# Performance work log

Measured on AMD Instinct MI355X. Metric: run time of the kernel, lower is better.

The kernel has to match this reference:

```python
import jax, jax.numpy as jnp
import numpy as np

S, B, V, E, H = 512, 256, 100000, 128, 256


def setup_inputs() -> dict:
    key = jax.random.key(0)
    k1, k2, k3, k4, k5, k6 = jax.random.split(key, 6)
    X = jax.random.randint(k1, (S, B), 0, V)
    emb = jax.random.normal(k2, (V, E), dtype=jnp.float32)
    # PyTorch nn.RNN init: U(-1/sqrt(H), 1/sqrt(H))
    s = 1.0 / np.sqrt(H)
    W_ih = jax.random.uniform(k3, (H, E), minval=-s, maxval=s, dtype=jnp.float32)
    W_hh = jax.random.uniform(k4, (H, H), minval=-s, maxval=s, dtype=jnp.float32)
    b_ih = jax.random.uniform(k5, (H,), minval=-s, maxval=s, dtype=jnp.float32)
    b_hh = jax.random.uniform(k6, (H,), minval=-s, maxval=s, dtype=jnp.float32)
    return {"X": X, "emb": emb, "W_ih": W_ih, "W_hh": W_hh, "b_ih": b_ih, "b_hh": b_hh}


def reference(X, emb, W_ih, W_hh, b_ih, b_hh):
    embedded = emb[X]                                   # [S, B, E]
    # Precompute input projections for all timesteps (one big GEMM)
    xproj = jnp.einsum('sbe,he->sbh', embedded, W_ih) + b_ih + b_hh  # [S, B, H]
    h0 = jnp.zeros((B, H), dtype=embedded.dtype)

    def step(h, xp):
        h_new = jnp.tanh(xp + h @ W_hh.T)
        return h_new, None

    h_last, _ = jax.lax.scan(step, h0, xproj)           # [B, H]
    return jax.nn.log_softmax(h_last, axis=1)
```

## Files before the change

kernel.cpp:

```cpp
#include <hip/hip_runtime.h>
#include <math.h>

#define S_LEN 512
#define B_SZ  256
#define E_SZ  128
#define H_SZ  256

typedef __attribute__((ext_vector_type(8))) short bf16x8;
typedef __attribute__((ext_vector_type(4))) short bf16x4;
typedef __attribute__((ext_vector_type(4))) float f32x4;

__device__ __forceinline__ short f2bf(float f) {
    union { float f; unsigned u; } v; v.f = f;
    unsigned r = v.u + 0x7FFFu + ((v.u >> 16) & 1u);
    return (short)(r >> 16);
}
__device__ __forceinline__ float bf2f(short h) {
    union { unsigned u; float f; } c;
    c.u = ((unsigned)(unsigned short)h) << 16;
    return c.f;
}

__device__ __forceinline__ float tanh_fast(float v) {
    float e = __expf(2.f * v);
    return 1.f - 2.f * __builtin_amdgcn_rcpf(e + 1.f);
}

__global__ __launch_bounds__(256, 2) void embed_proj_mfma(
    const int*   __restrict__ X,
    const float* __restrict__ emb,
    const float* __restrict__ W_ih,
    const float* __restrict__ b_ih,
    const float* __restrict__ b_hh,
    float*       __restrict__ xproj)
{
    __shared__ int   toks[64];
    __shared__ short BtH[4][4][64][8];
    __shared__ short BtL[4][4][64][8];

    const int tid  = threadIdx.x;
    const int wave = tid >> 6;
    const int lane = tid & 63;
    const int bl   = lane & 15;
    const int quad = lane >> 4;
    const size_t row0 = (size_t)blockIdx.x * 64;

    if (tid < 64) toks[tid] = X[row0 + tid];
    __syncthreads();

    {
        const int r  = tid >> 2;
        const int kk = tid & 3;
        const float* ep = emb + (size_t)toks[r] * E_SZ + kk * 32;
#pragma unroll
        for (int q = 0; q < 4; ++q) {
            float4 a = *(const float4*)(ep + q * 8);
            float4 b = *(const float4*)(ep + q * 8 + 4);
            float v[8] = {a.x, a.y, a.z, a.w, b.x, b.y, b.z, b.w};
            bf16x8 fh, fl;
#pragma unroll
            for (int j = 0; j < 8; ++j) {
                short h = f2bf(v[j]);
                fh[j] = h;
                fl[j] = f2bf(v[j] - bf2f(h));
            }
            *(bf16x8*)&BtH[r >> 4][kk][q * 16 + (r & 15)][0] = fh;
            *(bf16x8*)&BtL[r >> 4][kk][q * 16 + (r & 15)][0] = fl;
        }
    }
    __syncthreads();

#pragma unroll
    for (int mp = 0; mp < 2; ++mp) {
        bf16x8 wh[2][4], wl[2][4];
#pragma unroll
        for (int i = 0; i < 2; ++i) {
            const int h = wave * 64 + (mp * 2 + i) * 16 + bl;
#pragma unroll
            for (int kk = 0; kk < 4; ++kk) {
                const float* wp = W_ih + (size_t)h * E_SZ + kk * 32 + quad * 8;
                float4 a = *(const float4*)wp;
                float4 b = *(const float4*)(wp + 4);
                float v[8] = {a.x, a.y, a.z, a.w, b.x, b.y, b.z, b.w};
                bf16x8 fh, fl;
#pragma unroll
                for (int j = 0; j < 8; ++j) {
                    short hh = f2bf(v[j]);
                    fh[j] = hh;
                    fl[j] = f2bf(v[j] - bf2f(hh));
                }
                wh[i][kk] = fh; wl[i][kk] = fl;
            }
        }

        f32x4 acc[2][4];
#pragma unroll
        for (int i = 0; i < 2; ++i)
#pragma unroll
            for (int nt = 0; nt < 4; ++nt) acc[i][nt] = (f32x4){0.f, 0.f, 0.f, 0.f};

#pragma unroll
        for (int kk = 0; kk < 4; ++kk) {
            bf16x8 bh[4], blo[4];
#pragma unroll
            for (int nt = 0; nt < 4; ++nt) {
                bh[nt]  = *(const bf16x8*)&BtH[nt][kk][lane][0];
                blo[nt] = *(const bf16x8*)&BtL[nt][kk][lane][0];
            }
#pragma unroll
            for (int i = 0; i < 2; ++i)
#pragma unroll
                for (int nt = 0; nt < 4; ++nt) {
                    f32x4 a = acc[i][nt];
                    a = __builtin_amdgcn_mfma_f32_16x16x32_bf16(wh[i][kk], bh[nt],  a, 0, 0, 0);
                    a = __builtin_amdgcn_mfma_f32_16x16x32_bf16(wh[i][kk], blo[nt], a, 0, 0, 0);
                    a = __builtin_amdgcn_mfma_f32_16x16x32_bf16(wl[i][kk], bh[nt],  a, 0, 0, 0);
                    acc[i][nt] = a;
                }
        }

#pragma unroll
        for (int i = 0; i < 2; ++i) {
            const int hb = wave * 64 + (mp * 2 + i) * 16 + quad * 4;
            float4 bi = *(const float4*)&b_ih[hb];
            float4 bh4 = *(const float4*)&b_hh[hb];
#pragma unroll
            for (int nt = 0; nt < 4; ++nt) {
                f32x4 o = acc[i][nt];
                o[0] += bi.x + bh4.x; o[1] += bi.y + bh4.y;
                o[2] += bi.z + bh4.z; o[3] += bi.w + bh4.w;
                *(f32x4*)&xproj[(row0 + nt * 16 + bl) * H_SZ + hb] = o;
            }
        }
    }
}

__global__ __launch_bounds__(512) void rnn_scan_kernel(
    const float* __restrict__ xproj,
    const float* __restrict__ W_hh,
    float*       __restrict__ out)
{
    const int tid  = threadIdx.x;
    const int wave = tid >> 6;
    const int lane = tid & 63;
    const int bl   = lane & 15;
    const int quad = lane >> 4;
    const int B0   = blockIdx.x * 16;

    __shared__ short HB[2][8][64][8];
    __shared__ float sred[8][16];

    bf16x8 wfrag[2][8];
#pragma unroll
    for (int mt = 0; mt < 2; ++mt) {
        const int h = wave * 32 + mt * 16 + bl;
#pragma unroll
        for (int kk = 0; kk < 8; ++kk) {
            const float* wp = W_hh + (size_t)h * H_SZ + kk * 32 + quad * 8;
            float4 x0 = *(const float4*)wp;
            float4 x1 = *(const float4*)(wp + 4);
            bf16x8 f;
            f[0] = f2bf(x0.x); f[1] = f2bf(x0.y); f[2] = f2bf(x0.z); f[3] = f2bf(x0.w);
            f[4] = f2bf(x1.x); f[5] = f2bf(x1.y); f[6] = f2bf(x1.z); f[7] = f2bf(x1.w);
            wfrag[mt][kk] = f;
        }
    }

    short* const hb0 = &HB[0][0][0][0];
    short* const hb1 = &HB[1][0][0][0];

    ((int4*)hb0)[tid] = make_int4(0, 0, 0, 0);

    const short* rd0 = hb0 + lane * 8;
    const short* rd1 = hb1 + lane * 8;

    const int wo0 = wave * 512 + (quad >> 1) * 128 + bl * 8 + (quad & 1) * 4;
    const int wo1 = wo0 + 256;
    short* w0a = hb0 + wo0; short* w0b = hb0 + wo1;
    short* w1a = hb1 + wo0; short* w1b = hb1 + wo1;

    const size_t stp = (size_t)B_SZ * H_SZ;
    const float* xpb = xproj + (size_t)(B0 + bl) * H_SZ + wave * 32 + quad * 4;

    f32x4 xA0 = *(const f32x4*)(xpb);
    f32x4 xA1 = *(const f32x4*)(xpb + 16);
    f32x4 xB0 = *(const f32x4*)(xpb + stp);
    f32x4 xB1 = *(const f32x4*)(xpb + stp + 16);

    __syncthreads();

    float vf0[4], vf1[4];

    auto do_step = [&](const short* rd, short* wa, short* wb,
                       f32x4& x0, f32x4& x1, const float* pf) {
        bf16x8 bf[8];
#pragma unroll
        for (int kk = 0; kk < 8; ++kk)
            bf[kk] = *(const bf16x8*)(rd + kk * 512);

        f32x4 c0a = {0.f, 0.f, 0.f, 0.f}, c0b = {0.f, 0.f, 0.f, 0.f};
        f32x4 c1a = {0.f, 0.f, 0.f, 0.f}, c1b = {0.f, 0.f, 0.f, 0.f};
#pragma unroll
        for (int kk = 0; kk < 4; ++kk) {
            c0a = __builtin_amdgcn_mfma_f32_16x16x32_bf16(wfrag[0][kk],     bf[kk],     c0a, 0, 0, 0);
            c1a = __builtin_amdgcn_mfma_f32_16x16x32_bf16(wfrag[1][kk],     bf[kk],     c1a, 0, 0, 0);
            c0b = __builtin_amdgcn_mfma_f32_16x16x32_bf16(wfrag[0][kk + 4], bf[kk + 4], c0b, 0, 0, 0);
            c1b = __builtin_amdgcn_mfma_f32_16x16x32_bf16(wfrag[1][kk + 4], bf[kk + 4], c1b, 0, 0, 0);
        }
        const f32x4 d0 = c0a + c0b;
        const f32x4 d1 = c1a + c1b;

        float t0 = tanh_fast(d0[0] + x0[0]);
        float t1 = tanh_fast(d0[1] + x0[1]);
        float t2 = tanh_fast(d0[2] + x0[2]);
        float t3 = tanh_fast(d0[3] + x0[3]);
        float u0 = tanh_fast(d1[0] + x1[0]);
        float u1 = tanh_fast(d1[1] + x1[1]);
        float u2 = tanh_fast(d1[2] + x1[2]);
        float u3 = tanh_fast(d1[3] + x1[3]);
        unsigned p01, p23, q01, q23;
        asm("v_cvt_pk_bf16_f32 %0, %1, %2" : "=v"(p01) : "v"(t0), "v"(t1));
        asm("v_cvt_pk_bf16_f32 %0, %1, %2" : "=v"(p23) : "v"(t2), "v"(t3));
        asm("v_cvt_pk_bf16_f32 %0, %1, %2" : "=v"(q01) : "v"(u0), "v"(u1));
        asm("v_cvt_pk_bf16_f32 %0, %1, %2" : "=v"(q23) : "v"(u2), "v"(u3));
        *(uint2*)wa = make_uint2(p01, p23);
        *(uint2*)wb = make_uint2(q01, q23);

        x0 = *(const f32x4*)pf;
        x1 = *(const f32x4*)(pf + 16);

        asm volatile("s_waitcnt lgkmcnt(0)" ::: "memory");
        __builtin_amdgcn_sched_barrier(0);
        __builtin_amdgcn_s_barrier();
    };

    const float* pfA = xpb + 2 * stp;
    const float* pfB = xpb + 3 * stp;
    for (int s = 0; s < 510; s += 2) {
        do_step(rd0, w1a, w1b, xA0, xA1, pfA);
        do_step(rd1, w0a, w0b, xB0, xB1, pfB);
        pfA += 2 * stp; pfB += 2 * stp;
        if (pfA > xpb + 511 * stp) pfA = xpb;
        if (pfB > xpb + 511 * stp) pfB = xpb;
    }
    do_step(rd0, w1a, w1b, xA0, xA1, xpb);

    {
        bf16x8 bf[8];
#pragma unroll
        for (int kk = 0; kk < 8; ++kk)
            bf[kk] = *(const bf16x8*)(rd1 + kk * 512);
        f32x4 c0a = {0.f, 0.f, 0.f, 0.f}, c0b = {0.f, 0.f, 0.f, 0.f};
        f32x4 c1a = {0.f, 0.f, 0.f, 0.f}, c1b = {0.f, 0.f, 0.f, 0.f};
#pragma unroll
        for (int kk = 0; kk < 4; ++kk) {
            c0a = __builtin_amdgcn_mfma_f32_16x16x32_bf16(wfrag[0][kk],     bf[kk],     c0a, 0, 0, 0);
            c1a = __builtin_amdgcn_mfma_f32_16x16x32_bf16(wfrag[1][kk],     bf[kk],     c1a, 0, 0, 0);
            c0b = __builtin_amdgcn_mfma_f32_16x16x32_bf16(wfrag[0][kk + 4], bf[kk + 4], c0b, 0, 0, 0);
            c1b = __builtin_amdgcn_mfma_f32_16x16x32_bf16(wfrag[1][kk + 4], bf[kk + 4], c1b, 0, 0, 0);
        }
        const f32x4 d0 = c0a + c0b;
        const f32x4 d1 = c1a + c1b;
#pragma unroll
        for (int r = 0; r < 4; ++r) {
            vf0[r] = tanh_fast(d0[r] + xB0[r]);
            vf1[r] = tanh_fast(d1[r] + xB1[r]);
        }
    }

    float m = fmaxf(fmaxf(fmaxf(vf0[0], vf0[1]), fmaxf(vf0[2], vf0[3])),
                    fmaxf(fmaxf(vf1[0], vf1[1]), fmaxf(vf1[2], vf1[3])));
    m = fmaxf(m, __shfl_xor(m, 16));
    m = fmaxf(m, __shfl_xor(m, 32));
    if (lane < 16) sred[wave][bl] = m;
    __syncthreads();
    float mall = sred[0][bl];
#pragma unroll
    for (int w = 1; w < 8; ++w) mall = fmaxf(mall, sred[w][bl]);
    __syncthreads();

    float ss = 0.f;
#pragma unroll
    for (int r = 0; r < 4; ++r)
        ss += __expf(vf0[r] - mall) + __expf(vf1[r] - mall);
    ss += __shfl_xor(ss, 16);
    ss += __shfl_xor(ss, 32);
    if (lane < 16) sred[wave][bl] = ss;
    __syncthreads();
    float tot = sred[0][bl];
#pragma unroll
    for (int w = 1; w < 8; ++w) tot += sred[w][bl];
    const float lse = mall + __logf(tot);

    f32x4 o0, o1;
#pragma unroll
    for (int r = 0; r < 4; ++r) { o0[r] = vf0[r] - lse; o1[r] = vf1[r] - lse; }
    float* op = out + (size_t)(B0 + bl) * H_SZ + wave * 32 + quad * 4;
    *(f32x4*)op        = o0;
    *(f32x4*)(op + 16) = o1;
}

extern "C" void kernel_launch(void* const* d_in, const int* in_sizes, int n_in,
                              void* d_out, int out_size, void* d_ws, size_t ws_size,
                              hipStream_t stream) {
    const int*   X    = (const int*)  d_in[0];
    const float* emb  = (const float*)d_in[1];
    const float* W_ih = (const float*)d_in[2];
    const float* W_hh = (const float*)d_in[3];
    const float* b_ih = (const float*)d_in[4];
    const float* b_hh = (const float*)d_in[5];
    float* out   = (float*)d_out;
    float* xproj = (float*)d_ws;

    embed_proj_mfma<<<dim3((S_LEN * B_SZ) / 64), 256, 0, stream>>>(
        X, emb, W_ih, b_ih, b_hh, xproj);

    rnn_scan_kernel<<<dim3(B_SZ / 16), 512, 0, stream>>>(xproj, W_hh, out);
}
```

Baseline: 464.1 us.

## Pre-split W_ih to bf16 hi/lo, drop LDS staging, and halve scan block waves

```diff
diff --git a/kernel.cpp b/kernel.cpp
--- a/kernel.cpp
+++ b/kernel.cpp
@@ -7,18 +7,32 @@
 #define H_SZ  256
 
 typedef __attribute__((ext_vector_type(8))) short bf16x8;
-typedef __attribute__((ext_vector_type(4))) short bf16x4;
 typedef __attribute__((ext_vector_type(4))) float f32x4;
 
-__device__ __forceinline__ short f2bf(float f) {
-    union { float f; unsigned u; } v; v.f = f;
-    unsigned r = v.u + 0x7FFFu + ((v.u >> 16) & 1u);
-    return (short)(r >> 16);
-}
-__device__ __forceinline__ float bf2f(short h) {
-    union { unsigned u; float f; } c;
-    c.u = ((unsigned)(unsigned short)h) << 16;
-    return c.f;
+__device__ short g_wh[H_SZ * E_SZ];
+__device__ short g_wl[H_SZ * E_SZ];
+
+__device__ __forceinline__ unsigned pkbf(float a, float b) {
+    unsigned r; asm("v_cvt_pk_bf16_f32 %0, %1, %2" : "=v"(r) : "v"(a), "v"(b));
+    return r;
+}
+__device__ __forceinline__ float fromlo(unsigned u) {
+    union { unsigned u; float f; } c; c.u = u << 16; return c.f;
+}
+__device__ __forceinline__ float fromhi(unsigned u) {
+    union { unsigned u; float f; } c; c.u = u & 0xffff0000u; return c.f;
+}
+__device__ __forceinline__ void cvt_hilo8(float4 a, float4 b, bf16x8& hi, bf16x8& lo) {
+    unsigned h0 = pkbf(a.x, a.y), h1 = pkbf(a.z, a.w);
+    unsigned h2 = pkbf(b.x, b.y), h3 = pkbf(b.z, b.w);
+    unsigned l0 = pkbf(a.x - fromlo(h0), a.y - fromhi(h0));
+    unsigned l1 = pkbf(a.z - fromlo(h1), a.w - fromhi(h1));
+    unsigned l2 = pkbf(b.x - fromlo(h2), b.y - fromhi(h2));
+    unsigned l3 = pkbf(b.z - fromlo(h3), b.w - fromhi(h3));
+    union { bf16x8 v; unsigned u[4]; } H, L;
+    H.u[0] = h0; H.u[1] = h1; H.u[2] = h2; H.u[3] = h3;
+    L.u[0] = l0; L.u[1] = l1; L.u[2] = l2; L.u[3] = l3;
+    hi = H.v; lo = L.v;
 }
 
 __device__ __forceinline__ float tanh_fast(float v) {
@@ -26,18 +40,23 @@
     return 1.f - 2.f * __builtin_amdgcn_rcpf(e + 1.f);
 }
 
+__global__ void prep_w_kernel(const float* __restrict__ W_ih) {
+    const int i = (blockIdx.x * 256 + threadIdx.x) * 8;
+    float4 a = *(const float4*)&W_ih[i];
+    float4 b = *(const float4*)&W_ih[i + 4];
+    bf16x8 h, l;
+    cvt_hilo8(a, b, h, l);
+    *(bf16x8*)&g_wh[i] = h;
+    *(bf16x8*)&g_wl[i] = l;
+}
+
 __global__ __launch_bounds__(256, 2) void embed_proj_mfma(
     const int*   __restrict__ X,
     const float* __restrict__ emb,
-    const float* __restrict__ W_ih,
     const float* __restrict__ b_ih,
     const float* __restrict__ b_hh,
     float*       __restrict__ xproj)
 {
-    __shared__ int   toks[64];
-    __shared__ short BtH[4][4][64][8];
-    __shared__ short BtL[4][4][64][8];
-
     const int tid  = threadIdx.x;
     const int wave = tid >> 6;
     const int lane = tid & 63;
@@ -45,97 +64,68 @@
     const int quad = lane >> 4;
     const size_t row0 = (size_t)blockIdx.x * 64;
 
-    if (tid < 64) toks[tid] = X[row0 + tid];
-    __syncthreads();
-
-    {
-        const int r  = tid >> 2;
-        const int kk = tid & 3;
-        const float* ep = emb + (size_t)toks[r] * E_SZ + kk * 32;
-#pragma unroll
-        for (int q = 0; q < 4; ++q) {
-            float4 a = *(const float4*)(ep + q * 8);
-            float4 b = *(const float4*)(ep + q * 8 + 4);
-            float v[8] = {a.x, a.y, a.z, a.w, b.x, b.y, b.z, b.w};
-            bf16x8 fh, fl;
-#pragma unroll
-            for (int j = 0; j < 8; ++j) {
-                short h = f2bf(v[j]);
-                fh[j] = h;
-                fl[j] = f2bf(v[j] - bf2f(h));
+    int tok[4];
+#pragma unroll
+    for (int nt = 0; nt < 4; ++nt) tok[nt] = X[row0 + nt * 16 + bl];
+
+    bf16x8 wh[4][4], wl[4][4];
+#pragma unroll
+    for (int mt = 0; mt < 4; ++mt) {
+        const int off0 = (wave * 64 + mt * 16 + bl) * E_SZ + quad * 8;
+#pragma unroll
+        for (int kk = 0; kk < 4; ++kk) {
+            wh[mt][kk] = *(const bf16x8*)&g_wh[off0 + kk * 32];
+            wl[mt][kk] = *(const bf16x8*)&g_wl[off0 + kk * 32];
+        }
+    }
+
+    f32x4 bias[4];
+#pragma unroll
+    for (int mt = 0; mt < 4; ++mt) {
+        const int hb = wave * 64 + mt * 16 + quad * 4;
+        float4 bi = *(const float4*)&b_ih[hb];
+        float4 bh = *(const float4*)&b_hh[hb];
+        bias[mt][0] = bi.x + bh.x; bias[mt][1] = bi.y + bh.y;
+        bias[mt][2] = bi.z + bh.z; bias[mt][3] = bi.w + bh.w;
+    }
+
+#pragma unroll
+    for (int nt = 0; nt < 4; ++nt) {
+        const float* ep = emb + (size_t)tok[nt] * E_SZ + quad * 8;
+        bf16x8 bh8[4], bl8[4];
+#pragma unroll
+        for (int kk = 0; kk < 4; ++kk) {
+            float4 a = *(const float4*)(ep + kk * 32);
+            float4 b = *(const float4*)(ep + kk * 32 + 4);
+            cvt_hilo8(a, b, bh8[kk], bl8[kk]);
+        }
+
+        f32x4 acc[4];
+#pragma unroll
+        for (int mt = 0; mt < 4; ++mt) acc[mt] = (f32x4){0.f, 0.f, 0.f, 0.f};
+
+#pragma unroll
+        for (int kk = 0; kk < 4; ++kk)
+#pragma unroll
+            for (int mt = 0; mt < 4; ++mt) {
+                f32x4 a = acc[mt];
+                a = __builtin_amdgcn_mfma_f32_16x16x32_bf16(wh[mt][kk], bh8[kk], a, 0, 0, 0);
+                a = __builtin_amdgcn_mfma_f32_16x16x32_bf16(wh[mt][kk], bl8[kk], a, 0, 0, 0);
+                a = __builtin_amdgcn_mfma_f32_16x16x32_bf16(wl[mt][kk], bh8[kk], a, 0, 0, 0);
+                acc[mt] = a;
             }
-            *(bf16x8*)&BtH[r >> 4][kk][q * 16 + (r & 15)][0] = fh;
-            *(bf16x8*)&BtL[r >> 4][kk][q * 16 + (r & 15)][0] = fl;
-        }
-    }
-    __syncthreads();
-
-#pragma unroll
-    for (int mp = 0; mp < 2; ++mp) {
-        bf16x8 wh[2][4], wl[2][4];
-#pragma unroll
-        for (int i = 0; i < 2; ++i) {
-            const int h = wave * 64 + (mp * 2 + i) * 16 + bl;
-#pragma unroll
-            for (int kk = 0; kk < 4; ++kk) {
-                const float* wp = W_ih + (size_t)h * E_SZ + kk * 32 + quad * 8;
-                float4 a = *(const float4*)wp;
-                float4 b = *(const float4*)(wp + 4);
-                float v[8] = {a.x, a.y, a.z, a.w, b.x, b.y, b.z, b.w};
-                bf16x8 fh, fl;
-#pragma unroll
-                for (int j = 0; j < 8; ++j) {
-                    short hh = f2bf(v[j]);
-                    fh[j] = hh;
-                    fl[j] = f2bf(v[j] - bf2f(hh));
-                }
-                wh[i][kk] = fh; wl[i][kk] = fl;
-            }
-        }
-
-        f32x4 acc[2][4];
-#pragma unroll
-        for (int i = 0; i < 2; ++i)
-#pragma unroll
-            for (int nt = 0; nt < 4; ++nt) acc[i][nt] = (f32x4){0.f, 0.f, 0.f, 0.f};
-
-#pragma unroll
-        for (int kk = 0; kk < 4; ++kk) {
-            bf16x8 bh[4], blo[4];
-#pragma unroll
-            for (int nt = 0; nt < 4; ++nt) {
-                bh[nt]  = *(const bf16x8*)&BtH[nt][kk][lane][0];
-                blo[nt] = *(const bf16x8*)&BtL[nt][kk][lane][0];
-            }
-#pragma unroll
-            for (int i = 0; i < 2; ++i)
-#pragma unroll
-                for (int nt = 0; nt < 4; ++nt) {
-                    f32x4 a = acc[i][nt];
-                    a = __builtin_amdgcn_mfma_f32_16x16x32_bf16(wh[i][kk], bh[nt],  a, 0, 0, 0);
-                    a = __builtin_amdgcn_mfma_f32_16x16x32_bf16(wh[i][kk], blo[nt], a, 0, 0, 0);
-                    a = __builtin_amdgcn_mfma_f32_16x16x32_bf16(wl[i][kk], bh[nt],  a, 0, 0, 0);
-                    acc[i][nt] = a;
-                }
-        }
-
-#pragma unroll
-        for (int i = 0; i < 2; ++i) {
-            const int hb = wave * 64 + (mp * 2 + i) * 16 + quad * 4;
-            float4 bi = *(const float4*)&b_ih[hb];
-            float4 bh4 = *(const float4*)&b_hh[hb];
-#pragma unroll
-            for (int nt = 0; nt < 4; ++nt) {
-                f32x4 o = acc[i][nt];
-                o[0] += bi.x + bh4.x; o[1] += bi.y + bh4.y;
-                o[2] += bi.z + bh4.z; o[3] += bi.w + bh4.w;
-                *(f32x4*)&xproj[(row0 + nt * 16 + bl) * H_SZ + hb] = o;
-            }
-        }
-    }
-}
-
-__global__ __launch_bounds__(512) void rnn_scan_kernel(
+
+#pragma unroll
+        for (int mt = 0; mt < 4; ++mt) {
+            f32x4 o = acc[mt];
+            o[0] += bias[mt][0]; o[1] += bias[mt][1];
+            o[2] += bias[mt][2]; o[3] += bias[mt][3];
+            *(f32x4*)&xproj[(row0 + nt * 16 + bl) * H_SZ + wave * 64 + mt * 16 + quad * 4] = o;
+        }
+    }
+}
+
+__global__ __launch_bounds__(256, 1) void rnn_scan_kernel(
     const float* __restrict__ xproj,
     const float* __restrict__ W_hh,
     float*       __restrict__ out)
@@ -147,87 +137,94 @@
     const int quad = lane >> 4;
     const int B0   = blockIdx.x * 16;
 
-    __shared__ short HB[2][8][64][8];
-    __shared__ float sred[8][16];
-
-    bf16x8 wfrag[2][8];
-#pragma unroll
-    for (int mt = 0; mt < 2; ++mt) {
-        const int h = wave * 32 + mt * 16 + bl;
+    __shared__ short HB[2][4096];
+    __shared__ float sred[4][16];
+
+    bf16x8 wfrag[4][8];
+#pragma unroll
+    for (int mt = 0; mt < 4; ++mt) {
+        const int h = wave * 64 + mt * 16 + bl;
 #pragma unroll
         for (int kk = 0; kk < 8; ++kk) {
             const float* wp = W_hh + (size_t)h * H_SZ + kk * 32 + quad * 8;
-            float4 x0 = *(const float4*)wp;
-            float4 x1 = *(const float4*)(wp + 4);
-            bf16x8 f;
-            f[0] = f2bf(x0.x); f[1] = f2bf(x0.y); f[2] = f2bf(x0.z); f[3] = f2bf(x0.w);
-            f[4] = f2bf(x1.x); f[5] = f2bf(x1.y); f[6] = f2bf(x1.z); f[7] = f2bf(x1.w);
-            wfrag[mt][kk] = f;
-        }
-    }
-
-    short* const hb0 = &HB[0][0][0][0];
-    short* const hb1 = &HB[1][0][0][0];
-
-    ((int4*)hb0)[tid] = make_int4(0, 0, 0, 0);
+            float4 a = *(const float4*)wp;
+            float4 b = *(const float4*)(wp + 4);
+            union { bf16x8 v; unsigned u[4]; } F;
+            F.u[0] = pkbf(a.x, a.y); F.u[1] = pkbf(a.z, a.w);
+            F.u[2] = pkbf(b.x, b.y); F.u[3] = pkbf(b.z, b.w);
+            wfrag[mt][kk] = F.v;
+        }
+    }
+
+    short* const hb0 = HB[0];
+    short* const hb1 = HB[1];
+    ((int4*)hb0)[tid]       = make_int4(0, 0, 0, 0);
+    ((int4*)hb0)[tid + 256] = make_int4(0, 0, 0, 0);
 
     const short* rd0 = hb0 + lane * 8;
     const short* rd1 = hb1 + lane * 8;
 
-    const int wo0 = wave * 512 + (quad >> 1) * 128 + bl * 8 + (quad & 1) * 4;
-    const int wo1 = wo0 + 256;
-    short* w0a = hb0 + wo0; short* w0b = hb0 + wo1;
-    short* w1a = hb1 + wo0; short* w1b = hb1 + wo1;
+    const int wbase = wave * 1024 + (quad >> 1) * 128 + bl * 8 + (quad & 1) * 4;
+    short* const w0 = hb0 + wbase;
+    short* const w1 = hb1 + wbase;
 
     const size_t stp = (size_t)B_SZ * H_SZ;
-    const float* xpb = xproj + (size_t)(B0 + bl) * H_SZ + wave * 32 + quad * 4;
+    const float* xpb = xproj + (size_t)(B0 + bl) * H_SZ + wave * 64 + quad * 4;
 
     f32x4 xA0 = *(const f32x4*)(xpb);
     f32x4 xA1 = *(const f32x4*)(xpb + 16);
+    f32x4 xA2 = *(const f32x4*)(xpb + 32);
+    f32x4 xA3 = *(const f32x4*)(xpb + 48);
     f32x4 xB0 = *(const f32x4*)(xpb + stp);
     f32x4 xB1 = *(const f32x4*)(xpb + stp + 16);
+    f32x4 xB2 = *(const f32x4*)(xpb + stp + 32);
+    f32x4 xB3 = *(const f32x4*)(xpb + stp + 48);
 
     __syncthreads();
 
-    float vf0[4], vf1[4];
-
-    auto do_step = [&](const short* rd, short* wa, short* wb,
-                       f32x4& x0, f32x4& x1, const float* pf) {
+    auto do_step = [&](const short* rd, short* wr,
+                       f32x4& x0, f32x4& x1, f32x4& x2, f32x4& x3,
+                       const float* pf) {
         bf16x8 bf[8];
 #pragma unroll
         for (int kk = 0; kk < 8; ++kk)
             bf[kk] = *(const bf16x8*)(rd + kk * 512);
 
-        f32x4 c0a = {0.f, 0.f, 0.f, 0.f}, c0b = {0.f, 0.f, 0.f, 0.f};
-        f32x4 c1a = {0.f, 0.f, 0.f, 0.f}, c1b = {0.f, 0.f, 0.f, 0.f};
+        f32x4 ca0 = {0.f,0.f,0.f,0.f}, ca1 = {0.f,0.f,0.f,0.f};
+        f32x4 ca2 = {0.f,0.f,0.f,0.f}, ca3 = {0.f,0.f,0.f,0.f};
+        f32x4 cb0 = {0.f,0.f,0.f,0.f}, cb1 = {0.f,0.f,0.f,0.f};
+        f32x4 cb2 = {0.f,0.f,0.f,0.f}, cb3 = {0.f,0.f,0.f,0.f};
 #pragma unroll
         for (int kk = 0; kk < 4; ++kk) {
-            c0a = __builtin_amdgcn_mfma_f32_16x16x32_bf16(wfrag[0][kk],     bf[kk],     c0a, 0, 0, 0);
-            c1a = __builtin_amdgcn_mfma_f32_16x16x32_bf16(wfrag[1][kk],     bf[kk],     c1a, 0, 0, 0);
-            c0b = __builtin_amdgcn_mfma_f32_16x16x32_bf16(wfrag[0][kk + 4], bf[kk + 4], c0b, 0, 0, 0);
-            c1b = __builtin_amdgcn_mfma_f32_16x16x32_bf16(wfrag[1][kk + 4], bf[kk + 4], c1b, 0, 0, 0);
-        }
-        const f32x4 d0 = c0a + c0b;
-        const f32x4 d1 = c1a + c1b;
-
-        float t0 = tanh_fast(d0[0] + x0[0]);
-        float t1 = tanh_fast(d0[1] + x0[1]);
-        float t2 = tanh_fast(d0[2] + x0[2]);
-        float t3 = tanh_fast(d0[3] + x0[3]);
-        float u0 = tanh_fast(d1[0] + x1[0]);
-        float u1 = tanh_fast(d1[1] + x1[1]);
-        float u2 = tanh_fast(d1[2] + x1[2]);
-        float u3 = tanh_fast(d1[3] + x1[3]);
-        unsigned p01, p23, q01, q23;
-        asm("v_cvt_pk_bf16_f32 %0, %1, %2" : "=v"(p01) : "v"(t0), "v"(t1));
-        asm("v_cvt_pk_bf16_f32 %0, %1, %2" : "=v"(p23) : "v"(t2), "v"(t3));
-        asm("v_cvt_pk_bf16_f32 %0, %1, %2" : "=v"(q01) : "v"(u0), "v"(u1));
-        asm("v_cvt_pk_bf16_f32 %0, %1, %2" : "=v"(q23) : "v"(u2), "v"(u3));
-        *(uint2*)wa = make_uint2(p01, p23);
-        *(uint2*)wb = make_uint2(q01, q23);
+            ca0 = __builtin_amdgcn_mfma_f32_16x16x32_bf16(wfrag[0][kk],   bf[kk],   ca0, 0, 0, 0);
+            ca1 = __builtin_amdgcn_mfma_f32_16x16x32_bf16(wfrag[1][kk],   bf[kk],   ca1, 0, 0, 0);
+            ca2 = __builtin_amdgcn_mfma_f32_16x16x32_bf16(wfrag[2][kk],   bf[kk],   ca2, 0, 0, 0);
+            ca3 = __builtin_amdgcn_mfma_f32_16x16x32_bf16(wfrag[3][kk],   bf[kk],   ca3, 0, 0, 0);
+            cb0 = __builtin_amdgcn_mfma_f32_16x16x32_bf16(wfrag[0][kk+4], bf[kk+4], cb0, 0, 0, 0);
+            cb1 = __builtin_amdgcn_mfma_f32_16x16x32_bf16(wfrag[1][kk+4], bf[kk+4], cb1, 0, 0, 0);
+            cb2 = __builtin_amdgcn_mfma_f32_16x16x32_bf16(wfrag[2][kk+4], bf[kk+4], cb2, 0, 0, 0);
+            cb3 = __builtin_amdgcn_mfma_f32_16x16x32_bf16(wfrag[3][kk+4], bf[kk+4], cb3, 0, 0, 0);
+        }
+        const f32x4 d0 = ca0 + cb0, d1 = ca1 + cb1;
+        const f32x4 d2 = ca2 + cb2, d3 = ca3 + cb3;
+
+#define EPI(dd, xx, OFF) { \
+        float t0 = tanh_fast(dd[0] + xx[0]); \
+        float t1 = tanh_fast(dd[1] + xx[1]); \
+        float t2 = tanh_fast(dd[2] + xx[2]); \
+        float t3 = tanh_fast(dd[3] + xx[3]); \
+        unsigned pa = pkbf(t0, t1), pb = pkbf(t2, t3); \
+        *(uint2*)(wr + (OFF)) = make_uint2(pa, pb); }
+        EPI(d0, x0, 0)
+        EPI(d1, x1, 256)
+        EPI(d2, x2, 512)
+        EPI(d3, x3, 768)
+#undef EPI
 
         x0 = *(const f32x4*)pf;
         x1 = *(const f32x4*)(pf + 16);
+        x2 = *(const f32x4*)(pf + 32);
+        x3 = *(const f32x4*)(pf + 48);
 
         asm volatile("s_waitcnt lgkmcnt(0)" ::: "memory");
         __builtin_amdgcn_sched_barrier(0);
@@ -237,67 +234,79 @@
     const float* pfA = xpb + 2 * stp;
     const float* pfB = xpb + 3 * stp;
     for (int s = 0; s < 510; s += 2) {
-        do_step(rd0, w1a, w1b, xA0, xA1, pfA);
-        do_step(rd1, w0a, w0b, xB0, xB1, pfB);
+        do_step(rd0, w1, xA0, xA1, xA2, xA3, pfA);
+        do_step(rd1, w0, xB0, xB1, xB2, xB3, pfB);
         pfA += 2 * stp; pfB += 2 * stp;
         if (pfA > xpb + 511 * stp) pfA = xpb;
         if (pfB > xpb + 511 * stp) pfB = xpb;
     }
-    do_step(rd0, w1a, w1b, xA0, xA1, xpb);
-
+    do_step(rd0, w1, xA0, xA1, xA2, xA3, xpb);
+
+    float vf[4][4];
     {
         bf16x8 bf[8];
 #pragma unroll
         for (int kk = 0; kk < 8; ++kk)
             bf[kk] = *(const bf16x8*)(rd1 + kk * 512);
-        f32x4 c0a = {0.f, 0.f, 0.f, 0.f}, c0b = {0.f, 0.f, 0.f, 0.f};
-        f32x4 c1a = {0.f, 0.f, 0.f, 0.f}, c1b = {0.f, 0.f, 0.f, 0.f};
+        f32x4 ca0 = {0.f,0.f,0.f,0.f}, ca1 = {0.f,0.f,0.f,0.f};
+        f32x4 ca2 = {0.f,0.f,0.f,0.f}, ca3 = {0.f,0.f,0.f,0.f};
+        f32x4 cb0 = {0.f,0.f,0.f,0.f}, cb1 = {0.f,0.f,0.f,0.f};
+        f32x4 cb2 = {0.f,0.f,0.f,0.f}, cb3 = {0.f,0.f,0.f,0.f};
 #pragma unroll
         for (int kk = 0; kk < 4; ++kk) {
-            c0a = __builtin_amdgcn_mfma_f32_16x16x32_bf16(wfrag[0][kk],     bf[kk],     c0a, 0, 0, 0);
-            c1a = __builtin_amdgcn_mfma_f32_16x16x32_bf16(wfrag[1][kk],     bf[kk],     c1a, 0, 0, 0);
-            c0b = __builtin_amdgcn_mfma_f32_16x16x32_bf16(wfrag[0][kk + 4], bf[kk + 4], c0b, 0, 0, 0);
-            c1b = __builtin_amdgcn_mfma_f32_16x16x32_bf16(wfrag[1][kk + 4], bf[kk + 4], c1b, 0, 0, 0);
-        }
-        const f32x4 d0 = c0a + c0b;
-        const f32x4 d1 = c1a + c1b;
+            ca0 = __builtin_amdgcn_mfma_f32_16x16x32_bf16(wfrag[0][kk],   bf[kk],   ca0, 0, 0, 0);
+            ca1 = __builtin_amdgcn_mfma_f32_16x16x32_bf16(wfrag[1][kk],   bf[kk],   ca1, 0, 0, 0);
+            ca2 = __builtin_amdgcn_mfma_f32_16x16x32_bf16(wfrag[2][kk],   bf[kk],   ca2, 0, 0, 0);
+            ca3 = __builtin_amdgcn_mfma_f32_16x16x32_bf16(wfrag[3][kk],   bf[kk],   ca3, 0, 0, 0);
+            cb0 = __builtin_amdgcn_mfma_f32_16x16x32_bf16(wfrag[0][kk+4], bf[kk+4], cb0, 0, 0, 0);
+            cb1 = __builtin_amdgcn_mfma_f32_16x16x32_bf16(wfrag[1][kk+4], bf[kk+4], cb1, 0, 0, 0);
+            cb2 = __builtin_amdgcn_mfma_f32_16x16x32_bf16(wfrag[2][kk+4], bf[kk+4], cb2, 0, 0, 0);
+            cb3 = __builtin_amdgcn_mfma_f32_16x16x32_bf16(wfrag[3][kk+4], bf[kk+4], cb3, 0, 0, 0);
+        }
+        const f32x4 d0 = ca0 + cb0, d1 = ca1 + cb1;
+        const f32x4 d2 = ca2 + cb2, d3 = ca3 + cb3;
 #pragma unroll
         for (int r = 0; r < 4; ++r) {
-            vf0[r] = tanh_fast(d0[r] + xB0[r]);
-            vf1[r] = tanh_fast(d1[r] + xB1[r]);
-        }
-    }
-
-    float m = fmaxf(fmaxf(fmaxf(vf0[0], vf0[1]), fmaxf(vf0[2], vf0[3])),
-                    fmaxf(fmaxf(vf1[0], vf1[1]), fmaxf(vf1[2], vf1[3])));
+            vf[0][r] = tanh_fast(d0[r] + xB0[r]);
+            vf[1][r] = tanh_fast(d1[r] + xB1[r]);
+            vf[2][r] = tanh_fast(d2[r] + xB2[r]);
+            vf[3][r] = tanh_fast(d3[r] + xB3[r]);
+        }
+    }
+
+    float m = -1e30f;
+#pragma unroll
+    for (int mt = 0; mt < 4; ++mt)
+#pragma unroll
+        for (int r = 0; r < 4; ++r) m = fmaxf(m, vf[mt][r]);
     m = fmaxf(m, __shfl_xor(m, 16));
     m = fmaxf(m, __shfl_xor(m, 32));
     if (lane < 16) sred[wave][bl] = m;
     __syncthreads();
-    float mall = sred[0][bl];
-#pragma unroll
-    for (int w = 1; w < 8; ++w) mall = fmaxf(mall, sred[w][bl]);
+    const float mall = fmaxf(fmaxf(sred[0][bl], sred[1][bl]),
+                             fmaxf(sred[2][bl], sred[3][bl]));
     __syncthreads();
 
     float ss = 0.f;
 #pragma unroll
-    for (int r = 0; r < 4; ++r)
-        ss += __expf(vf0[r] - mall) + __expf(vf1[r] - mall);
+    for (int mt = 0; mt < 4; ++mt)
+#pragma unroll
+        for (int r = 0; r < 4; ++r) ss += __expf(vf[mt][r] - mall);
     ss += __shfl_xor(ss, 16);
     ss += __shfl_xor(ss, 32);
     if (lane < 16) sred[wave][bl] = ss;
     __syncthreads();
-    float tot = sred[0][bl];
-#pragma unroll
-    for (int w = 1; w < 8; ++w) tot += sred[w][bl];
+    const float tot = sred[0][bl] + sred[1][bl] + sred[2][bl] + sred[3][bl];
     const float lse = mall + __logf(tot);
 
-    f32x4 o0, o1;
-#pragma unroll
-    for (int r = 0; r < 4; ++r) { o0[r] = vf0[r] - lse; o1[r] = vf1[r] - lse; }
-    float* op = out + (size_t)(B0 + bl) * H_SZ + wave * 32 + quad * 4;
-    *(f32x4*)op        = o0;
-    *(f32x4*)(op + 16) = o1;
+    float* op = out + (size_t)(B0 + bl) * H_SZ + wave * 64 + quad * 4;
+#pragma unroll
+    for (int mt = 0; mt < 4; ++mt) {
+        f32x4 o;
+#pragma unroll
+        for (int r = 0; r < 4; ++r) o[r] = vf[mt][r] - lse;
+        *(f32x4*)(op + mt * 16) = o;
+    }
 }
 
 extern "C" void kernel_launch(void* const* d_in, const int* in_sizes, int n_in,
@@ -312,8 +321,8 @@
     float* out   = (float*)d_out;
     float* xproj = (float*)d_ws;
 
+    prep_w_kernel<<<dim3(16), 256, 0, stream>>>(W_ih);
     embed_proj_mfma<<<dim3((S_LEN * B_SZ) / 64), 256, 0, stream>>>(
-        X, emb, W_ih, b_ih, b_hh, xproj);
-
-    rnn_scan_kernel<<<dim3(B_SZ / 16), 512, 0, stream>>>(xproj, W_hh, out);
-}
+        X, emb, b_ih, b_hh, xproj);
+    rnn_scan_kernel<<<dim3(B_SZ / 16), 256, 0, stream>>>(xproj, W_hh, out);
+}
```

Result: slower. 557.9 us (+20.2%).

## Precompute bf16 hi/lo W_ih split, use packed converts, and shorten scan step chain

Applied to the files above, without the earlier changes.

```diff
diff --git a/kernel.cpp b/kernel.cpp
--- a/kernel.cpp
+++ b/kernel.cpp
@@ -7,29 +7,52 @@
 #define H_SZ  256
 
 typedef __attribute__((ext_vector_type(8))) short bf16x8;
-typedef __attribute__((ext_vector_type(4))) short bf16x4;
 typedef __attribute__((ext_vector_type(4))) float f32x4;
 
-__device__ __forceinline__ short f2bf(float f) {
-    union { float f; unsigned u; } v; v.f = f;
-    unsigned r = v.u + 0x7FFFu + ((v.u >> 16) & 1u);
-    return (short)(r >> 16);
-}
-__device__ __forceinline__ float bf2f(short h) {
-    union { unsigned u; float f; } c;
-    c.u = ((unsigned)(unsigned short)h) << 16;
-    return c.f;
-}
-
-__device__ __forceinline__ float tanh_fast(float v) {
-    float e = __expf(2.f * v);
-    return 1.f - 2.f * __builtin_amdgcn_rcpf(e + 1.f);
+__device__ short g_wh[H_SZ * E_SZ];
+__device__ short g_wl[H_SZ * E_SZ];
+
+__device__ __forceinline__ unsigned pkbf(float a, float b) {
+    unsigned r; asm("v_cvt_pk_bf16_f32 %0, %1, %2" : "=v"(r) : "v"(a), "v"(b));
+    return r;
+}
+__device__ __forceinline__ float fromlo(unsigned u) {
+    union { unsigned u; float f; } c; c.u = u << 16; return c.f;
+}
+__device__ __forceinline__ float fromhi(unsigned u) {
+    union { unsigned u; float f; } c; c.u = u & 0xffff0000u; return c.f;
+}
+__device__ __forceinline__ void cvt_hilo8(float4 a, float4 b, bf16x8& hi, bf16x8& lo) {
+    unsigned h0 = pkbf(a.x, a.y), h1 = pkbf(a.z, a.w);
+    unsigned h2 = pkbf(b.x, b.y), h3 = pkbf(b.z, b.w);
+    unsigned l0 = pkbf(a.x - fromlo(h0), a.y - fromhi(h0));
+    unsigned l1 = pkbf(a.z - fromlo(h1), a.w - fromhi(h1));
+    unsigned l2 = pkbf(b.x - fromlo(h2), b.y - fromhi(h2));
+    unsigned l3 = pkbf(b.z - fromlo(h3), b.w - fromhi(h3));
+    union { bf16x8 v; unsigned u[4]; } H, L;
+    H.u[0] = h0; H.u[1] = h1; H.u[2] = h2; H.u[3] = h3;
+    L.u[0] = l0; L.u[1] = l1; L.u[2] = l2; L.u[3] = l3;
+    hi = H.v; lo = L.v;
+}
+
+__device__ __forceinline__ float tanhC(float v) {
+    float e = __builtin_amdgcn_exp2f(v * 2.8853900818f);
+    return fmaf(-2.f, __builtin_amdgcn_rcpf(e + 1.f), 1.f);
+}
+
+__global__ void prep_w_kernel(const float* __restrict__ W_ih) {
+    const int i = (blockIdx.x * 256 + threadIdx.x) * 8;
+    float4 a = *(const float4*)&W_ih[i];
+    float4 b = *(const float4*)&W_ih[i + 4];
+    bf16x8 h, l;
+    cvt_hilo8(a, b, h, l);
+    *(bf16x8*)&g_wh[i] = h;
+    *(bf16x8*)&g_wl[i] = l;
 }
 
 __global__ __launch_bounds__(256, 2) void embed_proj_mfma(
     const int*   __restrict__ X,
     const float* __restrict__ emb,
-    const float* __restrict__ W_ih,
     const float* __restrict__ b_ih,
     const float* __restrict__ b_hh,
     float*       __restrict__ xproj)
@@ -56,14 +79,8 @@
         for (int q = 0; q < 4; ++q) {
             float4 a = *(const float4*)(ep + q * 8);
             float4 b = *(const float4*)(ep + q * 8 + 4);
-            float v[8] = {a.x, a.y, a.z, a.w, b.x, b.y, b.z, b.w};
             bf16x8 fh, fl;
-#pragma unroll
-            for (int j = 0; j < 8; ++j) {
-                short h = f2bf(v[j]);
-                fh[j] = h;
-                fl[j] = f2bf(v[j] - bf2f(h));
-            }
+            cvt_hilo8(a, b, fh, fl);
             *(bf16x8*)&BtH[r >> 4][kk][q * 16 + (r & 15)][0] = fh;
             *(bf16x8*)&BtL[r >> 4][kk][q * 16 + (r & 15)][0] = fl;
         }
@@ -75,21 +92,11 @@
         bf16x8 wh[2][4], wl[2][4];
 #pragma unroll
         for (int i = 0; i < 2; ++i) {
-            const int h = wave * 64 + (mp * 2 + i) * 16 + bl;
+            const int off0 = (wave * 64 + (mp * 2 + i) * 16 + bl) * E_SZ + quad * 8;
 #pragma unroll
             for (int kk = 0; kk < 4; ++kk) {
-                const float* wp = W_ih + (size_t)h * E_SZ + kk * 32 + quad * 8;
-                float4 a = *(const float4*)wp;
-                float4 b = *(const float4*)(wp + 4);
-                float v[8] = {a.x, a.y, a.z, a.w, b.x, b.y, b.z, b.w};
-                bf16x8 fh, fl;
-#pragma unroll
-                for (int j = 0; j < 8; ++j) {
-                    short hh = f2bf(v[j]);
-                    fh[j] = hh;
-                    fl[j] = f2bf(v[j] - bf2f(hh));
-                }
-                wh[i][kk] = fh; wl[i][kk] = fl;
+                wh[i][kk] = *(const bf16x8*)&g_wh[off0 + kk * 32];
+                wl[i][kk] = *(const bf16x8*)&g_wl[off0 + kk * 32];
             }
         }
 
@@ -122,7 +129,7 @@
 #pragma unroll
         for (int i = 0; i < 2; ++i) {
             const int hb = wave * 64 + (mp * 2 + i) * 16 + quad * 4;
-            float4 bi = *(const float4*)&b_ih[hb];
+            float4 bi  = *(const float4*)&b_ih[hb];
             float4 bh4 = *(const float4*)&b_hh[hb];
 #pragma unroll
             for (int nt = 0; nt < 4; ++nt) {
@@ -157,12 +164,12 @@
 #pragma unroll
         for (int kk = 0; kk < 8; ++kk) {
             const float* wp = W_hh + (size_t)h * H_SZ + kk * 32 + quad * 8;
-            float4 x0 = *(const float4*)wp;
-            float4 x1 = *(const float4*)(wp + 4);
-            bf16x8 f;
-            f[0] = f2bf(x0.x); f[1] = f2bf(x0.y); f[2] = f2bf(x0.z); f[3] = f2bf(x0.w);
-            f[4] = f2bf(x1.x); f[5] = f2bf(x1.y); f[6] = f2bf(x1.z); f[7] = f2bf(x1.w);
-            wfrag[mt][kk] = f;
+            float4 a = *(const float4*)wp;
+            float4 b = *(const float4*)(wp + 4);
+            union { bf16x8 v; unsigned u[4]; } F;
+            F.u[0] = pkbf(a.x, a.y); F.u[1] = pkbf(a.z, a.w);
+            F.u[2] = pkbf(b.x, b.y); F.u[3] = pkbf(b.z, b.w);
+            wfrag[mt][kk] = F.v;
         }
     }
 
@@ -189,8 +196,6 @@
 
     __syncthreads();
 
-    float vf0[4], vf1[4];
-
     auto do_step = [&](const short* rd, short* wa, short* wb,
                        f32x4& x0, f32x4& x1, const float* pf) {
         bf16x8 bf[8];
@@ -198,36 +203,40 @@
         for (int kk = 0; kk < 8; ++kk)
             bf[kk] = *(const bf16x8*)(rd + kk * 512);
 
-        f32x4 c0a = {0.f, 0.f, 0.f, 0.f}, c0b = {0.f, 0.f, 0.f, 0.f};
-        f32x4 c1a = {0.f, 0.f, 0.f, 0.f}, c1b = {0.f, 0.f, 0.f, 0.f};
-#pragma unroll
-        for (int kk = 0; kk < 4; ++kk) {
-            c0a = __builtin_amdgcn_mfma_f32_16x16x32_bf16(wfrag[0][kk],     bf[kk],     c0a, 0, 0, 0);
-            c1a = __builtin_amdgcn_mfma_f32_16x16x32_bf16(wfrag[1][kk],     bf[kk],     c1a, 0, 0, 0);
-            c0b = __builtin_amdgcn_mfma_f32_16x16x32_bf16(wfrag[0][kk + 4], bf[kk + 4], c0b, 0, 0, 0);
-            c1b = __builtin_amdgcn_mfma_f32_16x16x32_bf16(wfrag[1][kk + 4], bf[kk + 4], c1b, 0, 0, 0);
-        }
-        const f32x4 d0 = c0a + c0b;
-        const f32x4 d1 = c1a + c1b;
-
-        float t0 = tanh_fast(d0[0] + x0[0]);
-        float t1 = tanh_fast(d0[1] + x0[1]);
-        float t2 = tanh_fast(d0[2] + x0[2]);
-        float t3 = tanh_fast(d0[3] + x0[3]);
-        float u0 = tanh_fast(d1[0] + x1[0]);
-        float u1 = tanh_fast(d1[1] + x1[1]);
-        float u2 = tanh_fast(d1[2] + x1[2]);
-        float u3 = tanh_fast(d1[3] + x1[3]);
-        unsigned p01, p23, q01, q23;
-        asm("v_cvt_pk_bf16_f32 %0, %1, %2" : "=v"(p01) : "v"(t0), "v"(t1));
-        asm("v_cvt_pk_bf16_f32 %0, %1, %2" : "=v"(p23) : "v"(t2), "v"(t3));
-        asm("v_cvt_pk_bf16_f32 %0, %1, %2" : "=v"(q01) : "v"(u0), "v"(u1));
-        asm("v_cvt_pk_bf16_f32 %0, %1, %2" : "=v"(q23) : "v"(u2), "v"(u3));
-        *(uint2*)wa = make_uint2(p01, p23);
-        *(uint2*)wb = make_uint2(q01, q23);
-
-        x0 = *(const f32x4*)pf;
-        x1 = *(const f32x4*)(pf + 16);
+        f32x4 n0 = *(const f32x4*)pf;
+        f32x4 n1 = *(const f32x4*)(pf + 16);
+
+        f32x4 a0 = x0, a1 = x1;
+        f32x4 b0 = {0.f,0.f,0.f,0.f}, b1 = {0.f,0.f,0.f,0.f};
+        f32x4 c0 = {0.f,0.f,0.f,0.f}, c1 = {0.f,0.f,0.f,0.f};
+        f32x4 e0 = {0.f,0.f,0.f,0.f}, e1 = {0.f,0.f,0.f,0.f};
+        a0 = __builtin_amdgcn_mfma_f32_16x16x32_bf16(wfrag[0][0], bf[0], a0, 0, 0, 0);
+        a1 = __builtin_amdgcn_mfma_f32_16x16x32_bf16(wfrag[1][0], bf[0], a1, 0, 0, 0);
+        a0 = __builtin_amdgcn_mfma_f32_16x16x32_bf16(wfrag[0][1], bf[1], a0, 0, 0, 0);
+        a1 = __builtin_amdgcn_mfma_f32_16x16x32_bf16(wfrag[1][1], bf[1], a1, 0, 0, 0);
+        b0 = __builtin_amdgcn_mfma_f32_16x16x32_bf16(wfrag[0][2], bf[2], b0, 0, 0, 0);
+        b1 = __builtin_amdgcn_mfma_f32_16x16x32_bf16(wfrag[1][2], bf[2], b1, 0, 0, 0);
+        b0 = __builtin_amdgcn_mfma_f32_16x16x32_bf16(wfrag[0][3], bf[3], b0, 0, 0, 0);
+        b1 = __builtin_amdgcn_mfma_f32_16x16x32_bf16(wfrag[1][3], bf[3], b1, 0, 0, 0);
+        c0 = __builtin_amdgcn_mfma_f32_16x16x32_bf16(wfrag[0][4], bf[4], c0, 0, 0, 0);
+        c1 = __builtin_amdgcn_mfma_f32_16x16x32_bf16(wfrag[1][4], bf[4], c1, 0, 0, 0);
+        c0 = __builtin_amdgcn_mfma_f32_16x16x32_bf16(wfrag[0][5], bf[5], c0, 0, 0, 0);
+        c1 = __builtin_amdgcn_mfma_f32_16x16x32_bf16(wfrag[1][5], bf[5], c1, 0, 0, 0);
+        e0 = __builtin_amdgcn_mfma_f32_16x16x32_bf16(wfrag[0][6], bf[6], e0, 0, 0, 0);
+        e1 = __builtin_amdgcn_mfma_f32_16x16x32_bf16(wfrag[1][6], bf[6], e1, 0, 0, 0);
+        e0 = __builtin_amdgcn_mfma_f32_16x16x32_bf16(wfrag[0][7], bf[7], e0, 0, 0, 0);
+        e1 = __builtin_amdgcn_mfma_f32_16x16x32_bf16(wfrag[1][7], bf[7], e1, 0, 0, 0);
+        const f32x4 d0 = (a0 + b0) + (c0 + e0);
+        const f32x4 d1 = (a1 + b1) + (c1 + e1);
+
+        float t0 = tanhC(d0[0]), t1 = tanhC(d0[1]);
+        float t2 = tanhC(d0[2]), t3 = tanhC(d0[3]);
+        float u0 = tanhC(d1[0]), u1 = tanhC(d1[1]);
+        float u2 = tanhC(d1[2]), u3 = tanhC(d1[3]);
+        *(uint2*)wa = make_uint2(pkbf(t0, t1), pkbf(t2, t3));
+        *(uint2*)wb = make_uint2(pkbf(u0, u1), pkbf(u2, u3));
+
+        x0 = n0; x1 = n1;
 
         asm volatile("s_waitcnt lgkmcnt(0)" ::: "memory");
         __builtin_amdgcn_sched_barrier(0);
@@ -245,26 +254,33 @@
     }
     do_step(rd0, w1a, w1b, xA0, xA1, xpb);
 
+    float vf0[4], vf1[4];
     {
         bf16x8 bf[8];
 #pragma unroll
         for (int kk = 0; kk < 8; ++kk)
             bf[kk] = *(const bf16x8*)(rd1 + kk * 512);
-        f32x4 c0a = {0.f, 0.f, 0.f, 0.f}, c0b = {0.f, 0.f, 0.f, 0.f};
-        f32x4 c1a = {0.f, 0.f, 0.f, 0.f}, c1b = {0.f, 0.f, 0.f, 0.f};
-#pragma unroll
-        for (int kk = 0; kk < 4; ++kk) {
-            c0a = __builtin_amdgcn_mfma_f32_16x16x32_bf16(wfrag[0][kk],     bf[kk],     c0a, 0, 0, 0);
-            c1a = __builtin_amdgcn_mfma_f32_16x16x32_bf16(wfrag[1][kk],     bf[kk],     c1a, 0, 0, 0);
-            c0b = __builtin_amdgcn_mfma_f32_16x16x32_bf16(wfrag[0][kk + 4], bf[kk + 4], c0b, 0, 0, 0);
-            c1b = __builtin_amdgcn_mfma_f32_16x16x32_bf16(wfrag[1][kk + 4], bf[kk + 4], c1b, 0, 0, 0);
-        }
-        const f32x4 d0 = c0a + c0b;
-        const f32x4 d1 = c1a + c1b;
+        f32x4 a0 = xB0, a1 = xB1;
+        f32x4 b0 = {0.f,0.f,0.f,0.f}, b1 = {0.f,0.f,0.f,0.f};
+        f32x4 c0 = {0.f,0.f,0.f,0.f}, c1 = {0.f,0.f,0.f,0.f};
+        f32x4 e0 = {0.f,0.f,0.f,0.f}, e1 = {0.f,0.f,0.f,0.f};
+#pragma unroll
+        for (int kk = 0; kk < 2; ++kk) {
+            a0 = __builtin_amdgcn_mfma_f32_16x16x32_bf16(wfrag[0][kk],     bf[kk],     a0, 0, 0, 0);
+            a1 = __builtin_amdgcn_mfma_f32_16x16x32_bf16(wfrag[1][kk],     bf[kk],     a1, 0, 0, 0);
+            b0 = __builtin_amdgcn_mfma_f32_16x16x32_bf16(wfrag[0][kk + 2], bf[kk + 2], b0, 0, 0, 0);
+            b1 = __builtin_amdgcn_mfma_f32_16x16x32_bf16(wfrag[1][kk + 2], bf[kk + 2], b1, 0, 0, 0);
+            c0 = __builtin_amdgcn_mfma_f32_16x16x32_bf16(wfrag[0][kk + 4], bf[kk + 4], c0, 0, 0, 0);
+            c1 = __builtin_amdgcn_mfma_f32_16x16x32_bf16(wfrag[1][kk + 4], bf[kk + 4], c1, 0, 0, 0);
+            e0 = __builtin_amdgcn_mfma_f32_16x16x32_bf16(wfrag[0][kk + 6], bf[kk + 6], e0, 0, 0, 0);
+            e1 = __builtin_amdgcn_mfma_f32_16x16x32_bf16(wfrag[1][kk + 6], bf[kk + 6], e1, 0, 0, 0);
+        }
+        const f32x4 d0 = (a0 + b0) + (c0 + e0);
+        const f32x4 d1 = (a1 + b1) + (c1 + e1);
 #pragma unroll
         for (int r = 0; r < 4; ++r) {
-            vf0[r] = tanh_fast(d0[r] + xB0[r]);
-            vf1[r] = tanh_fast(d1[r] + xB1[r]);
+            vf0[r] = tanhC(d0[r]);
+            vf1[r] = tanhC(d1[r]);
         }
     }
 
@@ -312,8 +328,8 @@
     float* out   = (float*)d_out;
     float* xproj = (float*)d_ws;
 
+    prep_w_kernel<<<dim3(16), 256, 0, stream>>>(W_ih);
     embed_proj_mfma<<<dim3((S_LEN * B_SZ) / 64), 256, 0, stream>>>(
-        X, emb, W_ih, b_ih, b_hh, xproj);
-
+        X, emb, b_ih, b_hh, xproj);
     rnn_scan_kernel<<<dim3(B_SZ / 16), 512, 0, stream>>>(xproj, W_hh, out);
 }
```

Measured after the change: 542.8 us. +16.9%, slower.
